# Optimization experiments

Measured on AMD Instinct MI355X. Metric: run time of the kernel, lower is better.

## Reference

```python
import jax, jax.numpy as jnp
import numpy as np

D_MODEL = 1024
N_HEADS = 16
D_HEAD = D_MODEL // N_HEADS
D_FF = 4096
B, L = 4, 2048


def setup_inputs() -> dict:
    key = jax.random.key(0)
    ks = jax.random.split(key, 12)
    s = 0.02
    return {
        "x": jax.random.normal(ks[0], (B, L, D_MODEL), dtype=jnp.float32),
        "ln1_g": jnp.ones((D_MODEL,), jnp.float32),
        "ln1_b": jnp.zeros((D_MODEL,), jnp.float32),
        "w_qkv": jax.random.normal(ks[1], (D_MODEL, 3 * D_MODEL), jnp.float32) * s,
        "b_qkv": jnp.zeros((3 * D_MODEL,), jnp.float32),
        "w_out": jax.random.normal(ks[2], (D_MODEL, D_MODEL), jnp.float32) * s,
        "b_out": jnp.zeros((D_MODEL,), jnp.float32),
        "ln2_g": jnp.ones((D_MODEL,), jnp.float32),
        "ln2_b": jnp.zeros((D_MODEL,), jnp.float32),
        "w1": jax.random.normal(ks[3], (D_MODEL, D_FF), jnp.float32) * s,
        "b1": jnp.zeros((D_FF,), jnp.float32),
        "w2": jax.random.normal(ks[4], (D_FF, D_MODEL), jnp.float32) * s,
        "b2": jnp.zeros((D_MODEL,), jnp.float32),
    }


def _layernorm(x, g, b, eps=1e-5):
    mu = jnp.mean(x, axis=-1, keepdims=True)
    var = jnp.var(x, axis=-1, keepdims=True)
    return (x - mu) * jax.lax.rsqrt(var + eps) * g + b


def _attention(h, w_qkv, b_qkv, w_out, b_out):
    Bx, Lx, D = h.shape
    qkv = h @ w_qkv + b_qkv  # [B,L,3D]
    qkv = qkv.reshape(Bx, Lx, 3, N_HEADS, D_HEAD)
    q, k, v = qkv[:, :, 0], qkv[:, :, 1], qkv[:, :, 2]  # [B,L,H,Dh]
    att = jnp.einsum("bqhd,bkhd->bhqk", q, k) * (D_HEAD ** -0.5)
    causal = jnp.tril(jnp.ones((Lx, Lx), bool))
    att = jnp.where(causal, att, -jnp.inf)
    att = jax.nn.softmax(att, axis=-1)
    out = jnp.einsum("bhqk,bkhd->bqhd", att, v).reshape(Bx, Lx, D)
    return out @ w_out + b_out


def reference(x, ln1_g, ln1_b, w_qkv, b_qkv, w_out, b_out,
              ln2_g, ln2_b, w1, b1, w2, b2):
    h = x + _attention(_layernorm(x, ln1_g, ln1_b), w_qkv, b_qkv, w_out, b_out)
    ff = jax.nn.gelu(_layernorm(h, ln2_g, ln2_b) @ w1 + b1, approximate=False) @ w2 + b2
    return h + ff
```

## Files before the change

kernel.cpp:

```cpp
#include <hip/hip_runtime.h>
#include <hip/hip_bf16.h>


typedef float f32x4 __attribute__((ext_vector_type(4)));
typedef __bf16 bf16x8 __attribute__((ext_vector_type(8)));
typedef unsigned short u16;

#define MFMA16(a, b, c) __builtin_amdgcn_mfma_f32_16x16x32_bf16((a), (b), (c), 0, 0, 0)

#define GLL16(g, l)                                                            \
  __builtin_amdgcn_global_load_lds(                                            \
      (__attribute__((address_space(1))) void*)(g),                            \
      (__attribute__((address_space(3))) void*)(l), 16, 0, 0)

__device__ __forceinline__ u16 f2bf(float f) {
  union { float f; unsigned int u; } x; x.f = f;
  unsigned int r = x.u + 0x7fffu + ((x.u >> 16) & 1u);
  return (u16)(r >> 16);
}

__global__ __launch_bounds__(256) void ln_kernel(
    const float* __restrict__ x, const float* __restrict__ g,
    const float* __restrict__ b, u16* __restrict__ y)
{
  int row = blockIdx.x;
  int t = threadIdx.x;
  const float4* xr = (const float4*)(x + (size_t)row * 1024);
  float4 v = xr[t];
  float s  = v.x + v.y + v.z + v.w;
  float ss = v.x*v.x + v.y*v.y + v.z*v.z + v.w*v.w;
#pragma unroll
  for (int off = 1; off < 64; off <<= 1) {
    s  += __shfl_xor(s, off);
    ss += __shfl_xor(ss, off);
  }
  __shared__ float red[8];
  int w = t >> 6;
  if ((t & 63) == 0) { red[w*2] = s; red[w*2+1] = ss; }
  __syncthreads();
  s  = red[0] + red[2] + red[4] + red[6];
  ss = red[1] + red[3] + red[5] + red[7];
  float mu  = s * (1.0f / 1024.0f);
  float var = ss * (1.0f / 1024.0f) - mu * mu;
  float rs  = rsqrtf(var + 1e-5f);
  float4 gg = ((const float4*)g)[t];
  float4 bb = ((const float4*)b)[t];
  ushort4 o;
  o.x = f2bf((v.x - mu) * rs * gg.x + bb.x);
  o.y = f2bf((v.y - mu) * rs * gg.y + bb.y);
  o.z = f2bf((v.z - mu) * rs * gg.z + bb.z);
  o.w = f2bf((v.w - mu) * rs * gg.w + bb.w);
  ((ushort4*)y)[(size_t)row * 256 + t] = o;
}

__global__ __launch_bounds__(256) void wt_kernel(
    const float* __restrict__ W, u16* __restrict__ Wt, int K, int N)
{
  __shared__ u16 tile[32][33];
  int n0 = blockIdx.x * 32, k0 = blockIdx.y * 32;
  int t = threadIdx.x, tr = t >> 5, tc = t & 31;
#pragma unroll
  for (int i = 0; i < 4; ++i) {
    int k = k0 + tr + i * 8;
    tile[tc][tr + i * 8] = f2bf(W[(size_t)k * N + n0 + tc]);
  }
  __syncthreads();
#pragma unroll
  for (int i = 0; i < 4; ++i) {
    int n = n0 + tr + i * 8;
    Wt[(size_t)n * K + k0 + tc] = tile[tr + i * 8][tc];
  }
}

__global__ __launch_bounds__(256) void vt_kernel(
    const u16* __restrict__ qkv, u16* __restrict__ vt)
{
  __shared__ u16 tile[64][65];
  int bid = blockIdx.x;
  int lt = bid & 31, h = (bid >> 5) & 15, b = bid >> 9;
  int t = threadIdx.x;
  int tr = t >> 4, tc4 = (t & 15) * 4;
  const u16* src = qkv + ((size_t)(b * 2048 + lt * 64)) * 3072 + 2048 + h * 64;
#pragma unroll
  for (int i = 0; i < 4; ++i) {
    int ll = tr + i * 16;
    ushort4 v = *(const ushort4*)(src + (size_t)ll * 3072 + tc4);
    tile[ll][tc4] = v.x; tile[ll][tc4+1] = v.y; tile[ll][tc4+2] = v.z; tile[ll][tc4+3] = v.w;
  }
  __syncthreads();
  u16* dst = vt + ((size_t)(b * 16 + h) * 64) * 2048 + lt * 64;
#pragma unroll
  for (int i = 0; i < 4; ++i) {
    int d = tr + i * 16;
    ushort4 o;
    o.x = tile[tc4][d]; o.y = tile[tc4+1][d]; o.z = tile[tc4+2][d]; o.w = tile[tc4+3][d];
    *(ushort4*)(dst + (size_t)d * 2048 + tc4) = o;
  }
}

template<int GELU, int HAS_RES, int OUT_BF16>
__global__ __launch_bounds__(256, 2) void gemm_kernel(
    const u16* __restrict__ A, const u16* __restrict__ Bt,
    const float* __restrict__ bias, const float* __restrict__ res,
    void* __restrict__ Cout, int M, int N, int K)
{
  __shared__ u16 lA[2][128 * 32];
  __shared__ u16 lB[2][128 * 32];
  const int nbn = N >> 7;
  int nwg = gridDim.x;
  int wg = blockIdx.x;
  if ((nwg & 7) == 0) wg = (wg & 7) * (nwg >> 3) + (wg >> 3);
  int bm = wg / nbn, bn = wg % nbn;
  int tid = threadIdx.x;
  int w = tid >> 6, l = tid & 63;
  int lh = l & 15, lg = l >> 4;
  int wr = w >> 1, wc = w & 1;
  const size_t Kb = (size_t)K * 2;
  const char* Ab = (const char*)A + (size_t)(bm * 128) * Kb;
  const char* Bb = (const char*)Bt + (size_t)(bn * 128) * Kb;

  int c0 = w * 64 + l;
  int r0 = c0 >> 2, cb0 = (c0 & 3) << 4;
  int c1 = (4 + w) * 64 + l;
  int r1 = c1 >> 2, cb1 = (c1 & 3) << 4;

#define GSTAGE(sel, kt)                                                        \
  do {                                                                         \
    GLL16(Ab + (size_t)r0 * Kb + (size_t)(kt) * 64 + cb0,                      \
          (char*)lA[sel] + w * 1024);                                          \
    GLL16(Bb + (size_t)r0 * Kb + (size_t)(kt) * 64 + cb0,                      \
          (char*)lB[sel] + w * 1024);                                          \
    GLL16(Ab + (size_t)r1 * Kb + (size_t)(kt) * 64 + cb1,                      \
          (char*)lA[sel] + (4 + w) * 1024);                                    \
    GLL16(Bb + (size_t)r1 * Kb + (size_t)(kt) * 64 + cb1,                      \
          (char*)lB[sel] + (4 + w) * 1024);                                    \
  } while (0)

  f32x4 acc[4][4] = {};
  const int nkt = K >> 5;
  GSTAGE(0, 0);
  __syncthreads();
  int cur = 0;
  for (int kt = 0; kt < nkt; ++kt) {
    if (kt + 1 < nkt) GSTAGE(cur ^ 1, kt + 1);
    bf16x8 af[4], bfr[4];
#pragma unroll
    for (int m = 0; m < 4; ++m)
      af[m] = *(const bf16x8*)(lA[cur] + (wr * 64 + m * 16 + lh) * 32 + lg * 8);
#pragma unroll
    for (int n = 0; n < 4; ++n)
      bfr[n] = *(const bf16x8*)(lB[cur] + (wc * 64 + n * 16 + lh) * 32 + lg * 8);
#pragma unroll
    for (int m = 0; m < 4; ++m)
#pragma unroll
      for (int n = 0; n < 4; ++n)
        acc[m][n] = MFMA16(af[m], bfr[n], acc[m][n]);
    __syncthreads();
    cur ^= 1;
  }
#undef GSTAGE
#pragma unroll
  for (int m = 0; m < 4; ++m) {
    int row0 = bm * 128 + wr * 64 + m * 16 + lg * 4;
#pragma unroll
    for (int n = 0; n < 4; ++n) {
      int col = bn * 128 + wc * 64 + n * 16 + lh;
      float bv = bias[col];
#pragma unroll
      for (int r = 0; r < 4; ++r) {
        int row = row0 + r;
        float v = acc[m][n][r] + bv;
        if (GELU) v = 0.5f * v * (1.0f + erff(v * 0.70710678118f));
        if (HAS_RES) v += res[(size_t)row * N + col];
        if (OUT_BF16) ((u16*)Cout)[(size_t)row * N + col] = f2bf(v);
        else ((float*)Cout)[(size_t)row * N + col] = v;
      }
    }
  }
}

__global__ __launch_bounds__(256, 4) void attn_kernel(
    const u16* __restrict__ qkv, const u16* __restrict__ vt,
    u16* __restrict__ out)
{
  __shared__ u16 Ks[2][4096];
  __shared__ u16 Vs[2][4096];
  __shared__ u16 Ps[4][1024];

  const float C = 0.18033688011f;

  int bid = blockIdx.x;
  int pi = bid >> 6, bh = bid & 63;
  int b = bh >> 4, h = bh & 15;
  int tid = threadIdx.x;
  int w = tid >> 6, l = tid & 63;
  int lh = l & 15, lg = l >> 4;
  int lh7 = lh & 7;

  const char* kg = (const char*)qkv + (size_t)(b * 2048) * 6144 + 2048 + h * 128;
  const char* vg = (const char*)vt + (size_t)((b * 16 + h) * 64) * 4096;
  char* pbw = (char*)Ps[w] + lh * 128;

#pragma unroll 1
  for (int half = 0; half < 2; ++half) {
    int qb = half ? (31 - pi) : pi;
    int q0 = qb * 64 + w * 16;
    const u16* qbase = qkv + ((size_t)(b * 2048) + q0) * 3072 + h * 64;
    bf16x8 aq0 = *(const bf16x8*)(qbase + (size_t)lh * 3072 + lg * 8);
    bf16x8 aq1 = *(const bf16x8*)(qbase + (size_t)lh * 3072 + 32 + lg * 8);

    f32x4 o[4] = {};
    float m = -1e30f;
    float lsum = 0.f;
    int nt = qb + 1;

    __syncthreads();
#pragma unroll
    for (int i = 0; i < 2; ++i) {
      int u = tid + i * 256;
      int row = u >> 3, uc = u & 7, sw = uc ^ (row & 7);
      GLL16(kg + (size_t)row * 6144 + sw * 16,
            (char*)Ks[0] + (size_t)(i * 256 + w * 64) * 16);
      GLL16(vg + (size_t)row * 4096 + sw * 16,
            (char*)Vs[0] + (size_t)(i * 256 + w * 64) * 16);
    }

#pragma unroll 1
    for (int kt = 0; kt < nt; ++kt) {
      int cur = kt & 1;
      __syncthreads();
      if (kt + 1 < nt) {
        int nxt = cur ^ 1;
        size_t kofs = (size_t)(kt + 1) * 64;
#pragma unroll
        for (int i = 0; i < 2; ++i) {
          int u = tid + i * 256;
          int row = u >> 3, uc = u & 7, sw = uc ^ (row & 7);
          GLL16(kg + (kofs + row) * 6144 + sw * 16,
                (char*)Ks[nxt] + (size_t)(i * 256 + w * 64) * 16);
          GLL16(vg + (size_t)row * 4096 + kofs * 2 + sw * 16,
                (char*)Vs[nxt] + (size_t)(i * 256 + w * 64) * 16);
        }
      }
      const char* kbuf = (const char*)Ks[cur];
      f32x4 s[4];
#pragma unroll
      for (int kb = 0; kb < 4; ++kb) {
        int row = kb * 16 + lh;
        const char* rp = kbuf + row * 128;
        bf16x8 a0 = *(const bf16x8*)(rp + ((lg ^ lh7) << 4));
        bf16x8 a1 = *(const bf16x8*)(rp + (((4 + lg) ^ lh7) << 4));
        f32x4 z = {0.f, 0.f, 0.f, 0.f};
        z = MFMA16(a0, aq0, z);
        z = MFMA16(a1, aq1, z);
        s[kb] = z;
      }
      if (kt == qb) {
        int qin = w * 16 + lh;
#pragma unroll
        for (int kb = 0; kb < 4; ++kb)
#pragma unroll
          for (int r = 0; r < 4; ++r)
            if (kb * 16 + lg * 4 + r > qin) s[kb][r] = -1e30f;
      }
      float tm = fmaxf(fmaxf(s[0][0], s[0][1]), fmaxf(s[0][2], s[0][3]));
#pragma unroll
      for (int kb = 1; kb < 4; ++kb)
        tm = fmaxf(tm, fmaxf(fmaxf(s[kb][0], s[kb][1]), fmaxf(s[kb][2], s[kb][3])));
      tm = fmaxf(tm, __shfl_xor(tm, 16));
      tm = fmaxf(tm, __shfl_xor(tm, 32));
      if (__any(tm > m + 64.0f)) {
        float nm = fmaxf(m, tm);
        float f = __builtin_amdgcn_exp2f((m - nm) * C);
        m = nm; lsum *= f;
#pragma unroll
        for (int db = 0; db < 4; ++db)
#pragma unroll
          for (int r = 0; r < 4; ++r) o[db][r] *= f;
      }
      float mc = m * C;
      float ps = 0.f;
#pragma unroll
      for (int kb = 0; kb < 4; ++kb)
#pragma unroll
        for (int r = 0; r < 4; ++r) {
          float p = __builtin_amdgcn_exp2f(fmaf(s[kb][r], C, -mc));
          s[kb][r] = p;
          ps += p;
        }
      ps += __shfl_xor(ps, 16);
      ps += __shfl_xor(ps, 32);
      lsum += ps;
#pragma unroll
      for (int kb = 0; kb < 4; ++kb) {
        unsigned lo, hi;
        asm("v_cvt_pk_bf16_f32 %0, %1, %2" : "=v"(lo) : "v"(s[kb][0]), "v"(s[kb][1]));
        asm("v_cvt_pk_bf16_f32 %0, %1, %2" : "=v"(hi) : "v"(s[kb][2]), "v"(s[kb][3]));
        int unit = kb * 2 + (lg >> 1);
        uint2 val; val.x = lo; val.y = hi;
        *(uint2*)(pbw + ((unit ^ lh7) << 4) + ((lg & 1) << 3)) = val;
      }
      bf16x8 pa0 = *(const bf16x8*)(pbw + ((lg ^ lh7) << 4));
      bf16x8 pa1 = *(const bf16x8*)(pbw + (((4 + lg) ^ lh7) << 4));
      const char* vbuf = (const char*)Vs[cur];
#pragma unroll
      for (int db = 0; db < 4; ++db) {
        int row = db * 16 + lh;
        const char* rp = vbuf + row * 128;
        bf16x8 v0 = *(const bf16x8*)(rp + ((lg ^ lh7) << 4));
        bf16x8 v1 = *(const bf16x8*)(rp + (((4 + lg) ^ lh7) << 4));
        o[db] = MFMA16(v0, pa0, o[db]);
        o[db] = MFMA16(v1, pa1, o[db]);
      }
    }
    float rinv = 1.0f / lsum;
    u16* ob = out + ((size_t)(b * 2048) + q0 + lh) * 1024 + h * 64;
#pragma unroll
    for (int db = 0; db < 4; ++db) {
      ushort4 pk;
      pk.x = f2bf(o[db][0] * rinv);
      pk.y = f2bf(o[db][1] * rinv);
      pk.z = f2bf(o[db][2] * rinv);
      pk.w = f2bf(o[db][3] * rinv);
      *(ushort4*)(ob + db * 16 + lg * 4) = pk;
    }
  }
}

extern "C" void kernel_launch(void* const* d_in, const int* in_sizes, int n_in,
                              void* d_out, int out_size, void* d_ws, size_t ws_size,
                              hipStream_t stream) {
  const float* x     = (const float*)d_in[0];
  const float* ln1_g = (const float*)d_in[1];
  const float* ln1_b = (const float*)d_in[2];
  const float* w_qkv = (const float*)d_in[3];
  const float* b_qkv = (const float*)d_in[4];
  const float* w_out = (const float*)d_in[5];
  const float* b_out = (const float*)d_in[6];
  const float* ln2_g = (const float*)d_in[7];
  const float* ln2_b = (const float*)d_in[8];
  const float* w1    = (const float*)d_in[9];
  const float* b1    = (const float*)d_in[10];
  const float* w2    = (const float*)d_in[11];
  const float* b2    = (const float*)d_in[12];

  char* ws = (char*)d_ws;
  u16* wqkvT = (u16*)(ws + 0);
  u16* woutT = (u16*)(ws + 6291456);
  u16* w1T   = (u16*)(ws + 8388608);
  u16* w2T   = (u16*)(ws + 16777216);
  u16* qkv   = (u16*)(ws + 25165824);
  u16* ffn1  = (u16*)(ws + 25165824);
  u16* vtb   = (u16*)(ws + 75497472);
  u16* lnb   = (u16*)(ws + 92274688);
  u16* attn  = lnb;
  float* h   = (float*)(ws + 125829120);

  wt_kernel<<<dim3(96, 32), 256, 0, stream>>>(w_qkv, wqkvT, 1024, 3072);
  wt_kernel<<<dim3(32, 32), 256, 0, stream>>>(w_out, woutT, 1024, 1024);
  wt_kernel<<<dim3(128, 32), 256, 0, stream>>>(w1, w1T, 1024, 4096);
  wt_kernel<<<dim3(32, 128), 256, 0, stream>>>(w2, w2T, 4096, 1024);

  ln_kernel<<<8192, 256, 0, stream>>>(x, ln1_g, ln1_b, lnb);
  gemm_kernel<0, 0, 1><<<1536, 256, 0, stream>>>(lnb, wqkvT, b_qkv, nullptr, qkv, 8192, 3072, 1024);
  vt_kernel<<<2048, 256, 0, stream>>>(qkv, vtb);
  attn_kernel<<<1024, 256, 0, stream>>>(qkv, vtb, attn);
  gemm_kernel<0, 1, 0><<<512, 256, 0, stream>>>(attn, woutT, b_out, x, h, 8192, 1024, 1024);
  ln_kernel<<<8192, 256, 0, stream>>>(h, ln2_g, ln2_b, lnb);
  gemm_kernel<1, 0, 1><<<2048, 256, 0, stream>>>(lnb, w1T, b1, nullptr, ffn1, 8192, 4096, 1024);
  gemm_kernel<0, 1, 0><<<512, 256, 0, stream>>>(ffn1, w2T, b2, h, (float*)d_out, 8192, 1024, 4096);
}
```

Measured before the change: 406.8 us.

## Replace GEMM with 8-wave 256-row tiles, 4-stage LDS pipeline and swizzle

Replaces the 128x128, 4-wave double-buffered GEMM with a 512-thread kernel that computes 256xBN tiles (BN=256 or 128), using a 4-deep LDS ring prefetched three k-steps ahead, XOR-swizzled LDS layout, explicit vmcnt/lgkmcnt waits, and s_setprio around the MFMA bursts. The goal is more reuse per loaded tile, better hiding of global-to-LDS latency, and fewer LDS bank conflicts across all four GEMMs. In exchange it uses far more LDS and accumulator registers per block, and the grids become smaller, which can leave CUs underfilled on the N=1024 GEMMs.

```diff
diff --git a/kernel.cpp b/kernel.cpp
--- a/kernel.cpp
+++ b/kernel.cpp
@@ -12,6 +12,14 @@
   __builtin_amdgcn_global_load_lds(                                            \
       (__attribute__((address_space(1))) void*)(g),                            \
       (__attribute__((address_space(3))) void*)(l), 16, 0, 0)
+
+#define BAR()                                                                  \
+  do {                                                                         \
+    __builtin_amdgcn_sched_barrier(0);                                         \
+    __builtin_amdgcn_s_barrier();                                              \
+    asm volatile("" ::: "memory");                                             \
+    __builtin_amdgcn_sched_barrier(0);                                         \
+  } while (0)
 
 __device__ __forceinline__ u16 f2bf(float f) {
   union { float f; unsigned int u; } x; x.f = f;
@@ -98,77 +106,126 @@
   }
 }
 
-template<int GELU, int HAS_RES, int OUT_BF16>
-__global__ __launch_bounds__(256, 2) void gemm_kernel(
+template<int NF, int GELU, int HAS_RES, int OUT_BF16>
+__global__ __launch_bounds__(512, 2) void gemm8_kernel(
     const u16* __restrict__ A, const u16* __restrict__ Bt,
     const float* __restrict__ bias, const float* __restrict__ res,
     void* __restrict__ Cout, int M, int N, int K)
 {
-  __shared__ u16 lA[2][128 * 32];
-  __shared__ u16 lB[2][128 * 32];
-  const int nbn = N >> 7;
-  int nwg = gridDim.x;
-  int wg = blockIdx.x;
+  constexpr int BN = NF * 64;
+  constexpr int BUFU = (256 + BN) * 32;
+  __shared__ u16 lds[4][BUFU];
+
+  const int nbn = N / BN;
+  int nwg = gridDim.x, wg = blockIdx.x;
   if ((nwg & 7) == 0) wg = (wg & 7) * (nwg >> 3) + (wg >> 3);
-  int bm = wg / nbn, bn = wg % nbn;
-  int tid = threadIdx.x;
-  int w = tid >> 6, l = tid & 63;
-  int lh = l & 15, lg = l >> 4;
-  int wr = w >> 1, wc = w & 1;
+  const int bm = wg / nbn, bn = wg % nbn;
+  const int tid = threadIdx.x;
+  const int l = tid & 63;
+  const int lh = l & 15, lg = l >> 4;
+  const int w = tid >> 6;
+  const int wr = w >> 2, wc = w & 3;
+
   const size_t Kb = (size_t)K * 2;
-  const char* Ab = (const char*)A + (size_t)(bm * 128) * Kb;
-  const char* Bb = (const char*)Bt + (size_t)(bn * 128) * Kb;
-
-  int c0 = w * 64 + l;
-  int r0 = c0 >> 2, cb0 = (c0 & 3) << 4;
-  int c1 = (4 + w) * 64 + l;
-  int r1 = c1 >> 2, cb1 = (c1 & 3) << 4;
-
-#define GSTAGE(sel, kt)                                                        \
+  const char* Ab = (const char*)A + (size_t)(bm * 256) * Kb;
+  const char* Bb = (const char*)Bt + (size_t)(bn * BN) * Kb;
+
+  const int swst = ((tid ^ (tid >> 3)) & 3) << 4;
+  const size_t stA = (size_t)(tid >> 2) * Kb + swst;
+
+  const int swo = ((lg ^ (lh >> 1)) & 3) << 4;
+  const int offA0 = (wr * 128 + lh) * 64 + swo;
+  const int offB0 = (wc * NF * 16 + lh) * 64 + swo;
+
+#define STAGE_A8(kt, dst)                                                      \
   do {                                                                         \
-    GLL16(Ab + (size_t)r0 * Kb + (size_t)(kt) * 64 + cb0,                      \
-          (char*)lA[sel] + w * 1024);                                          \
-    GLL16(Bb + (size_t)r0 * Kb + (size_t)(kt) * 64 + cb0,                      \
-          (char*)lB[sel] + w * 1024);                                          \
-    GLL16(Ab + (size_t)r1 * Kb + (size_t)(kt) * 64 + cb1,                      \
-          (char*)lA[sel] + (4 + w) * 1024);                                    \
-    GLL16(Bb + (size_t)r1 * Kb + (size_t)(kt) * 64 + cb1,                      \
-          (char*)lB[sel] + (4 + w) * 1024);                                    \
+    GLL16(Ab + stA + (size_t)(kt) * 64, (dst) + tid * 16);                     \
+    GLL16(Ab + stA + 128 * Kb + (size_t)(kt) * 64, (dst) + tid * 16 + 8192);   \
   } while (0)
-
-  f32x4 acc[4][4] = {};
+#define STAGE_B8(kt, dst)                                                      \
+  do {                                                                         \
+    GLL16(Bb + stA + (size_t)(kt) * 64, (dst) + tid * 16);                     \
+    if (NF == 4)                                                               \
+      GLL16(Bb + stA + 128 * Kb + (size_t)(kt) * 64, (dst) + tid * 16 + 8192); \
+  } while (0)
+
+  {
+    char* d0 = (char*)lds[0]; STAGE_A8(0, d0); STAGE_B8(0, d0 + 16384);
+    char* d1 = (char*)lds[1]; STAGE_A8(1, d1); STAGE_B8(1, d1 + 16384);
+    char* d2 = (char*)lds[2]; STAGE_A8(2, d2); STAGE_B8(2, d2 + 16384);
+  }
+  if (NF == 4) asm volatile("s_waitcnt vmcnt(8)" ::: "memory");
+  else         asm volatile("s_waitcnt vmcnt(6)" ::: "memory");
+  BAR();
+
+  f32x4 acc[8][NF] = {};
   const int nkt = K >> 5;
-  GSTAGE(0, 0);
-  __syncthreads();
-  int cur = 0;
-  for (int kt = 0; kt < nkt; ++kt) {
-    if (kt + 1 < nkt) GSTAGE(cur ^ 1, kt + 1);
-    bf16x8 af[4], bfr[4];
+#pragma unroll 1
+  for (int t = 0; t < nkt; ++t) {
+    const char* bufA = (const char*)lds[t & 3];
+    const char* bufB = bufA + 16384;
+    char* sdst = (char*)lds[(t + 3) & 3];
+    const bool st = (t + 3 < nkt);
+    bf16x8 af[4], bf[NF];
 #pragma unroll
     for (int m = 0; m < 4; ++m)
-      af[m] = *(const bf16x8*)(lA[cur] + (wr * 64 + m * 16 + lh) * 32 + lg * 8);
-#pragma unroll
-    for (int n = 0; n < 4; ++n)
-      bfr[n] = *(const bf16x8*)(lB[cur] + (wc * 64 + n * 16 + lh) * 32 + lg * 8);
+      af[m] = *(const bf16x8*)(bufA + offA0 + m * 1024);
+#pragma unroll
+    for (int n = 0; n < NF; ++n)
+      bf[n] = *(const bf16x8*)(bufB + offB0 + n * 1024);
+    if (st) STAGE_A8(t + 3, sdst);
+    BAR();
+    asm volatile("s_waitcnt lgkmcnt(0)" ::: "memory");
+    __builtin_amdgcn_sched_barrier(0);
+    __builtin_amdgcn_s_setprio(1);
 #pragma unroll
     for (int m = 0; m < 4; ++m)
 #pragma unroll
-      for (int n = 0; n < 4; ++n)
-        acc[m][n] = MFMA16(af[m], bfr[n], acc[m][n]);
-    __syncthreads();
-    cur ^= 1;
-  }
-#undef GSTAGE
-#pragma unroll
-  for (int m = 0; m < 4; ++m) {
-    int row0 = bm * 128 + wr * 64 + m * 16 + lg * 4;
-#pragma unroll
-    for (int n = 0; n < 4; ++n) {
-      int col = bn * 128 + wc * 64 + n * 16 + lh;
-      float bv = bias[col];
+      for (int n = 0; n < NF; ++n)
+        acc[m][n] = MFMA16(af[m], bf[n], acc[m][n]);
+    __builtin_amdgcn_s_setprio(0);
+    BAR();
+#pragma unroll
+    for (int m = 0; m < 4; ++m)
+      af[m] = *(const bf16x8*)(bufA + offA0 + 4096 + m * 1024);
+    if (st) STAGE_B8(t + 3, sdst + 16384);
+    BAR();
+    asm volatile("s_waitcnt lgkmcnt(0)" ::: "memory");
+    __builtin_amdgcn_sched_barrier(0);
+    __builtin_amdgcn_s_setprio(1);
+#pragma unroll
+    for (int m = 0; m < 4; ++m)
+#pragma unroll
+      for (int n = 0; n < NF; ++n)
+        acc[4 + m][n] = MFMA16(af[m], bf[n], acc[4 + m][n]);
+    __builtin_amdgcn_s_setprio(0);
+    __builtin_amdgcn_sched_barrier(0);
+    if (t < nkt - 1) {
+      if (t <= nkt - 4) {
+        if (NF == 4) asm volatile("s_waitcnt vmcnt(8)" ::: "memory");
+        else         asm volatile("s_waitcnt vmcnt(6)" ::: "memory");
+      } else if (t == nkt - 3) {
+        if (NF == 4) asm volatile("s_waitcnt vmcnt(4)" ::: "memory");
+        else         asm volatile("s_waitcnt vmcnt(3)" ::: "memory");
+      } else {
+        asm volatile("s_waitcnt vmcnt(0)" ::: "memory");
+      }
+      BAR();
+    }
+  }
+#undef STAGE_A8
+#undef STAGE_B8
+
+#pragma unroll
+  for (int m = 0; m < 8; ++m) {
+    const int row0 = bm * 256 + wr * 128 + m * 16 + lg * 4;
+#pragma unroll
+    for (int n = 0; n < NF; ++n) {
+      const int col = bn * BN + wc * NF * 16 + n * 16 + lh;
+      const float bv = bias[col];
 #pragma unroll
       for (int r = 0; r < 4; ++r) {
-        int row = row0 + r;
+        const int row = row0 + r;
         float v = acc[m][n][r] + bv;
         if (GELU) v = 0.5f * v * (1.0f + erff(v * 0.70710678118f));
         if (HAS_RES) v += res[(size_t)row * N + col];
@@ -177,6 +234,7 @@
       }
     }
   }
+  (void)M;
 }
 
 __global__ __launch_bounds__(256, 4) void attn_kernel(
@@ -362,11 +420,11 @@
   wt_kernel<<<dim3(32, 128), 256, 0, stream>>>(w2, w2T, 4096, 1024);
 
   ln_kernel<<<8192, 256, 0, stream>>>(x, ln1_g, ln1_b, lnb);
-  gemm_kernel<0, 0, 1><<<1536, 256, 0, stream>>>(lnb, wqkvT, b_qkv, nullptr, qkv, 8192, 3072, 1024);
+  gemm8_kernel<4, 0, 0, 1><<<384, 512, 0, stream>>>(lnb, wqkvT, b_qkv, nullptr, qkv, 8192, 3072, 1024);
   vt_kernel<<<2048, 256, 0, stream>>>(qkv, vtb);
   attn_kernel<<<1024, 256, 0, stream>>>(qkv, vtb, attn);
-  gemm_kernel<0, 1, 0><<<512, 256, 0, stream>>>(attn, woutT, b_out, x, h, 8192, 1024, 1024);
+  gemm8_kernel<2, 0, 1, 0><<<256, 512, 0, stream>>>(attn, woutT, b_out, x, h, 8192, 1024, 1024);
   ln_kernel<<<8192, 256, 0, stream>>>(h, ln2_g, ln2_b, lnb);
-  gemm_kernel<1, 0, 1><<<2048, 256, 0, stream>>>(lnb, w1T, b1, nullptr, ffn1, 8192, 4096, 1024);
-  gemm_kernel<0, 1, 0><<<512, 256, 0, stream>>>(ffn1, w2T, b2, h, (float*)d_out, 8192, 1024, 4096);
-}
+  gemm8_kernel<4, 1, 0, 1><<<512, 512, 0, stream>>>(lnb, w1T, b1, nullptr, ffn1, 8192, 4096, 1024);
+  gemm8_kernel<2, 0, 1, 0><<<256, 512, 0, stream>>>(ffn1, w2T, b2, h, (float*)d_out, 8192, 1024, 4096);
+}
```

After: 408.5 us. About the same (+0.4%).

## Triple-buffer GEMM LDS with swizzled layout and fine-grained vmcnt waits

Applied to the files above, without the earlier changes.

The GEMM main loop moves from double to triple buffering. Loads for tile t+2 are issued after the LDS fragment reads, and the per-iteration __syncthreads is replaced by a partial s_waitcnt vmcnt plus s_barrier, so two global-to-LDS loads stay in flight. The source column chunk is XOR-swizzled so the 16-byte fragment reads avoid LDS bank conflicts, and s_setprio raises priority around the MFMA block. The extra LDS buffer can reduce occupancy, and the hand-written waitcnt counts must match the four loads issued per stage.

```diff
diff --git a/kernel.cpp b/kernel.cpp
--- a/kernel.cpp
+++ b/kernel.cpp
@@ -104,8 +104,8 @@
     const float* __restrict__ bias, const float* __restrict__ res,
     void* __restrict__ Cout, int M, int N, int K)
 {
-  __shared__ u16 lA[2][128 * 32];
-  __shared__ u16 lB[2][128 * 32];
+  __shared__ u16 lA[3][128 * 32];
+  __shared__ u16 lB[3][128 * 32];
   const int nbn = N >> 7;
   int nwg = gridDim.x;
   int wg = blockIdx.x;
@@ -120,45 +120,66 @@
   const char* Bb = (const char*)Bt + (size_t)(bn * 128) * Kb;
 
   int c0 = w * 64 + l;
-  int r0 = c0 >> 2, cb0 = (c0 & 3) << 4;
+  int r0 = c0 >> 2, sw0 = ((c0 ^ (c0 >> 3)) & 3) << 4;
   int c1 = (4 + w) * 64 + l;
-  int r1 = c1 >> 2, cb1 = (c1 & 3) << 4;
+  int r1 = c1 >> 2, sw1 = ((c1 ^ (c1 >> 3)) & 3) << 4;
 
 #define GSTAGE(sel, kt)                                                        \
   do {                                                                         \
-    GLL16(Ab + (size_t)r0 * Kb + (size_t)(kt) * 64 + cb0,                      \
+    GLL16(Ab + (size_t)r0 * Kb + (size_t)(kt) * 64 + sw0,                      \
           (char*)lA[sel] + w * 1024);                                          \
-    GLL16(Bb + (size_t)r0 * Kb + (size_t)(kt) * 64 + cb0,                      \
+    GLL16(Bb + (size_t)r0 * Kb + (size_t)(kt) * 64 + sw0,                      \
           (char*)lB[sel] + w * 1024);                                          \
-    GLL16(Ab + (size_t)r1 * Kb + (size_t)(kt) * 64 + cb1,                      \
+    GLL16(Ab + (size_t)r1 * Kb + (size_t)(kt) * 64 + sw1,                      \
           (char*)lA[sel] + (4 + w) * 1024);                                    \
-    GLL16(Bb + (size_t)r1 * Kb + (size_t)(kt) * 64 + cb1,                      \
+    GLL16(Bb + (size_t)r1 * Kb + (size_t)(kt) * 64 + sw1,                      \
           (char*)lB[sel] + (4 + w) * 1024);                                    \
   } while (0)
+
+  const int swo = ((lg ^ (lh >> 1)) & 3) << 4;
+  const int offA = (wr * 64 + lh) * 64 + swo;
+  const int offB = (wc * 64 + lh) * 64 + swo;
 
   f32x4 acc[4][4] = {};
   const int nkt = K >> 5;
   GSTAGE(0, 0);
-  __syncthreads();
-  int cur = 0;
-  for (int kt = 0; kt < nkt; ++kt) {
-    if (kt + 1 < nkt) GSTAGE(cur ^ 1, kt + 1);
+  GSTAGE(1, 1);
+  asm volatile("s_waitcnt vmcnt(4)" ::: "memory");
+  __builtin_amdgcn_s_barrier();
+  __builtin_amdgcn_sched_barrier(0);
+
+  int cur = 0, s2 = 2;
+#pragma unroll 1
+  for (int t = 0; t < nkt; ++t) {
+    const char* bufA = (const char*)lA[cur];
+    const char* bufB = (const char*)lB[cur];
     bf16x8 af[4], bfr[4];
 #pragma unroll
     for (int m = 0; m < 4; ++m)
-      af[m] = *(const bf16x8*)(lA[cur] + (wr * 64 + m * 16 + lh) * 32 + lg * 8);
+      af[m] = *(const bf16x8*)(bufA + offA + m * 1024);
 #pragma unroll
     for (int n = 0; n < 4; ++n)
-      bfr[n] = *(const bf16x8*)(lB[cur] + (wc * 64 + n * 16 + lh) * 32 + lg * 8);
+      bfr[n] = *(const bf16x8*)(bufB + offB + n * 1024);
+    if (t + 2 < nkt) GSTAGE(s2, t + 2);
+    __builtin_amdgcn_s_setprio(1);
 #pragma unroll
     for (int m = 0; m < 4; ++m)
 #pragma unroll
       for (int n = 0; n < 4; ++n)
         acc[m][n] = MFMA16(af[m], bfr[n], acc[m][n]);
-    __syncthreads();
-    cur ^= 1;
+    __builtin_amdgcn_s_setprio(0);
+    if (t < nkt - 1) {
+      __builtin_amdgcn_sched_barrier(0);
+      if (t < nkt - 2) asm volatile("s_waitcnt vmcnt(4)" ::: "memory");
+      else             asm volatile("s_waitcnt vmcnt(0)" ::: "memory");
+      __builtin_amdgcn_s_barrier();
+      __builtin_amdgcn_sched_barrier(0);
+    }
+    cur = (cur == 2) ? 0 : cur + 1;
+    s2  = (s2 == 2) ? 0 : s2 + 1;
   }
 #undef GSTAGE
+
 #pragma unroll
   for (int m = 0; m < 4; ++m) {
     int row0 = bm * 128 + wr * 64 + m * 16 + lg * 4;
@@ -177,6 +198,7 @@
       }
     }
   }
+  (void)M;
 }
 
 __global__ __launch_bounds__(256, 4) void attn_kernel(
```

New measurement: 390.8 us. 1.04x faster.
